# Performance work log

Measured on AMD Instinct MI355X. Metric: run time of the kernel, lower is better.

Reference implementation:

```python
import jax, jax.numpy as jnp
import numpy as np

B = 4; S_L = 512; WIN = 256; SCH = 3; CCH = 128; F = 8; P = 4; RNN = 128; FC = 256
L1 = (WIN - F + 1) // P          # after conv1 + pool1
L2 = (L1 - F + 1) // P           # after conv2 + pool2
D1 = L2 * CCH                    # flattened conv feature dim fed to GRU


def _conv1d(x, w, b):
    # x: (N, W, Cin), w: (F, Cin, Cout), VALID, stride 1 (matches keras Conv1D)
    return jax.lax.conv_general_dilated(x, w, (1,), 'VALID', dimension_numbers=('NWC', 'WIO', 'NWC')) + b


def _maxpool(x, p):
    return jax.lax.reduce_window(x, -jnp.inf, jax.lax.max, (1, p, 1), (1, p, 1), 'VALID')


def _gru(x, h0, mask, W, U, b):
    # keras GRU v2 (reset_after=True). b[0]=input bias, b[1]=recurrent bias.
    # Masked steps carry state through (keras semantics: output==state for GRU).
    u = U.shape[0]
    xg = x @ W + b[0]  # (B, T, 3u) precomputed input projections
    br = b[1]

    def step(h, inp):
        xt, mt = inp  # (B, 3u), (B,)
        rg = h @ U + br
        z = jax.nn.sigmoid(xt[:, :u] + rg[:, :u])
        r = jax.nn.sigmoid(xt[:, u:2 * u] + rg[:, u:2 * u])
        hh = jnp.tanh(xt[:, 2 * u:] + r * rg[:, 2 * u:])
        hn = z * h + (1.0 - z) * hh
        hn = jnp.where(mt[:, None], hn, h)
        return hn, hn

    _, ys = jax.lax.scan(step, h0, (jnp.swapaxes(xg, 0, 1), jnp.swapaxes(mask, 0, 1)))
    return jnp.swapaxes(ys, 0, 1)  # (B, T, u)


def _bidir(x, m, hf, hb, Wf, Uf, bf, Wb, Ub, bb):
    # Bidirectional(merge='concat'); backward layer sees reversed inputs+mask,
    # its output is reversed back to align with time (keras behaviour).
    yf = _gru(x, hf, m, Wf, Uf, bf)
    yb = _gru(x[:, ::-1], hb, m[:, ::-1], Wb, Ub, bb)[:, ::-1]
    return jnp.concatenate([yf, yb], axis=-1)


def _forward(x, state1_f, state1_b, state2_f, state2_b,
             conv1_w, conv1_b, conv2_w, conv2_b,
             g1f_W, g1f_U, g1f_b, g1b_W, g1b_U, g1b_b,
             g2f_W, g2f_U, g2f_b, g2b_W, g2b_U, g2b_b,
             d1_w, d1_b, d2_w, d2_b, d3_w, d3_b, m):
    bsz = x.shape[0]
    h = x.reshape(bsz * S_L, WIN, SCH)
    h = _maxpool(jax.nn.leaky_relu(_conv1d(h, conv1_w, conv1_b), 0.2), P)
    h = _maxpool(jax.nn.leaky_relu(_conv1d(h, conv2_w, conv2_b), 0.2), P)
    h = h.reshape(bsz, S_L, D1)
    h = _bidir(h, m, state1_f, state1_b, g1f_W, g1f_U, g1f_b, g1b_W, g1b_U, g1b_b)
    h = _bidir(h, m, state2_f, state2_b, g2f_W, g2f_U, g2f_b, g2b_W, g2b_U, g2b_b)
    # keras layers.Attention(use_scale=False): dot-product self attention,
    # key mask -> -1e9 on scores, query mask -> zero outputs.
    scores = jnp.einsum('btd,bsd->bts', h, h)
    scores = jnp.where(m[:, None, :], scores, -1e9)
    h = jnp.einsum('bts,bsd->btd', jax.nn.softmax(scores, axis=-1), h)
    h = h * m[:, :, None].astype(h.dtype)
    h = jax.nn.leaky_relu(h @ d1_w + d1_b, 0.2)   # dropout is identity at inference
    h = jax.nn.leaky_relu(h @ d2_w + d2_b, 0.2)
    return (h @ d3_w + d3_b)[..., 0]              # squeeze -> (B, s_l)


def setup_inputs() -> dict:
    key = jax.random.key(0)
    ks = jax.random.split(key, 32)
    g = lambda k, s: jax.random.normal(k, s, jnp.float32) * 0.05
    inp = {}
    inp['x'] = jax.random.normal(ks[0], (B, S_L, WIN, SCH), jnp.float32)
    inp['m'] = jax.random.randint(ks[1], (B, S_L), 0, 2) > 0
    inp['state1_f'] = jax.random.uniform(ks[2], (B, RNN), jnp.float32, -1.0, 1.0)
    inp['state1_b'] = jax.random.uniform(ks[3], (B, RNN), jnp.float32, -1.0, 1.0)
    inp['state2_f'] = jax.random.uniform(ks[4], (B, RNN), jnp.float32, -1.0, 1.0)
    inp['state2_b'] = jax.random.uniform(ks[5], (B, RNN), jnp.float32, -1.0, 1.0)
    inp['conv1_w'] = g(ks[6], (F, SCH, CCH)); inp['conv1_b'] = jnp.zeros((CCH,), jnp.float32)
    inp['conv2_w'] = g(ks[7], (F, CCH, CCH)); inp['conv2_b'] = jnp.zeros((CCH,), jnp.float32)
    i = 8
    for nm, din in (('g1f', D1), ('g1b', D1), ('g2f', 2 * RNN), ('g2b', 2 * RNN)):
        inp[nm + '_W'] = g(ks[i], (din, 3 * RNN))
        inp[nm + '_U'] = g(ks[i + 1], (RNN, 3 * RNN))
        inp[nm + '_b'] = jnp.zeros((2, 3 * RNN), jnp.float32)
        i += 2
    inp['d1_w'] = g(ks[i], (2 * RNN, FC)); inp['d1_b'] = jnp.zeros((FC,), jnp.float32)
    inp['d2_w'] = g(ks[i + 1], (FC, FC)); inp['d2_b'] = jnp.zeros((FC,), jnp.float32)
    inp['d3_w'] = g(ks[i + 2], (FC, 1)); inp['d3_b'] = jnp.zeros((1,), jnp.float32)
    return inp


def reference(x, m, state1_f, state1_b, state2_f, state2_b,
              conv1_w, conv1_b, conv2_w, conv2_b,
              g1f_W, g1f_U, g1f_b, g1b_W, g1b_U, g1b_b,
              g2f_W, g2f_U, g2f_b, g2b_W, g2b_U, g2b_b,
              d1_w, d1_b, d2_w, d2_b, d3_w, d3_b):
    return _forward(x, state1_f, state1_b, state2_f, state2_b,
                    conv1_w, conv1_b, conv2_w, conv2_b,
                    g1f_W, g1f_U, g1f_b, g1b_W, g1b_U, g1b_b,
                    g2f_W, g2f_U, g2f_b, g2b_W, g2b_U, g2b_b,
                    d1_w, d1_b, d2_w, d2_b, d3_w, d3_b, m)
```

## Files before the change

kernel.cpp:

```cpp
#include <hip/hip_runtime.h>

#define LRELU(v) ((v) > 0.f ? (v) : 0.2f * (v))

typedef float f32x4 __attribute__((ext_vector_type(4)));
typedef __bf16 bf16x8 __attribute__((ext_vector_type(8)));
typedef unsigned short ushort8v __attribute__((ext_vector_type(8)));
typedef unsigned int u32x2 __attribute__((ext_vector_type(2)));

__device__ __forceinline__ unsigned short f2bf(float f) {
    unsigned int u = __float_as_uint(f);
    u += 0x7fffu + ((u >> 16) & 1u);
    return (unsigned short)(u >> 16);
}
__device__ __forceinline__ float bf2f(unsigned short h) {
    return __uint_as_float(((unsigned int)h) << 16);
}
__device__ __forceinline__ float sigmoid_fast(float x) {
    float e = __builtin_amdgcn_exp2f(-x * 1.442695041f);
    return __builtin_amdgcn_rcpf(1.f + e);
}
__device__ __forceinline__ float tanh_fast(float x) {
    float e = __builtin_amdgcn_exp2f(x * 2.885390082f);
    return 1.f - 2.f * __builtin_amdgcn_rcpf(e + 1.f);
}
__device__ __forceinline__ float dpp_add_xor1(float v) {
    int r = __builtin_amdgcn_mov_dpp(__float_as_int(v), 0xB1, 0xF, 0xF, true);
    return v + __int_as_float(r);
}
__device__ __forceinline__ float dpp_add_xor2(float v) {
    int r = __builtin_amdgcn_mov_dpp(__float_as_int(v), 0x4E, 0xF, 0xF, true);
    return v + __int_as_float(r);
}

__device__ __forceinline__ void wtpack(const float* __restrict__ W,
                                       unsigned short* __restrict__ h,
                                       unsigned short* __restrict__ l, int K,
                                       int N, long idx) {
    int n = (int)(idx / K), k = (int)(idx % K);
    float v = W[(long)k * N + n];
    unsigned short hi = f2bf(v);
    h[idx] = hi;
    l[idx] = f2bf(v - bf2f(hi));
}
__device__ __forceinline__ void ugpack(const float* __restrict__ U,
                                       float* __restrict__ up, int widx) {
    int quad = widx >> 11;
    int rem = widx & 2047;
    int t = rem >> 2, i = rem & 3;
    int g = quad >> 3, q = quad & 7;
    int c = t >> 2, kq = t & 3;
    up[widx] = U[(long)(kq * 32 + q * 4 + i) * 384 + g * 128 + c];
}

__global__ __launch_bounds__(256) void prepack_all(
    const float* __restrict__ w2, unsigned short* __restrict__ bth,
    unsigned short* __restrict__ btl, const float* __restrict__ g1fW,
    unsigned short* __restrict__ wt1fh, unsigned short* __restrict__ wt1fl,
    const float* __restrict__ g1bW, unsigned short* __restrict__ wt1bh,
    unsigned short* __restrict__ wt1bl, const float* __restrict__ g2fW,
    unsigned short* __restrict__ wt2fh, unsigned short* __restrict__ wt2fl,
    const float* __restrict__ g2bW, unsigned short* __restrict__ wt2bh,
    unsigned short* __restrict__ wt2bl, const float* __restrict__ g1fU,
    float* __restrict__ up1f, const float* __restrict__ g1bU,
    float* __restrict__ up1b, const float* __restrict__ g2fU,
    float* __restrict__ up2f, const float* __restrict__ g2bU,
    float* __restrict__ up2b, const unsigned int* __restrict__ mraw,
    int* __restrict__ mi) {
    const int bid = blockIdx.x, tid = threadIdx.x;
    if (bid < 512) {
        int idx = bid * 256 + tid;
        int c = idx >> 10, k = idx & 1023;
        float v = w2[k * 128 + c];
        unsigned short hi = f2bf(v);
        bth[(long)c * 1024 + k] = hi;
        btl[(long)c * 1024 + k] = f2bf(v - bf2f(hi));
    } else if (bid < 3008) {
        wtpack(g1fW, wt1fh, wt1fl, 1664, 384, (long)(bid - 512) * 256 + tid);
    } else if (bid < 5504) {
        wtpack(g1bW, wt1bh, wt1bl, 1664, 384, (long)(bid - 3008) * 256 + tid);
    } else if (bid < 5888) {
        wtpack(g2fW, wt2fh, wt2fl, 256, 384, (long)(bid - 5504) * 256 + tid);
    } else if (bid < 6272) {
        wtpack(g2bW, wt2bh, wt2bl, 256, 384, (long)(bid - 5888) * 256 + tid);
    } else if (bid < 6464) {
        ugpack(g1fU, up1f, (bid - 6272) * 256 + tid);
    } else if (bid < 6656) {
        ugpack(g1bU, up1b, (bid - 6464) * 256 + tid);
    } else if (bid < 6848) {
        ugpack(g2fU, up2f, (bid - 6656) * 256 + tid);
    } else if (bid < 7040) {
        ugpack(g2bU, up2b, (bid - 6848) * 256 + tid);
    } else {
        __shared__ int flag;
        if (tid == 0) flag = 0;
        __syncthreads();
        unsigned a = mraw[tid * 2], bb = mraw[tid * 2 + 1];
        if (a > 1u || bb > 1u) flag = 1;
        __syncthreads();
        if (flag) {
            const unsigned char* b8 = (const unsigned char*)mraw;
            for (int i = tid; i < 2048; i += 256) mi[i] = b8[i] ? 1 : 0;
        } else {
            for (int i = tid; i < 2048; i += 256) mi[i] = mraw[i] ? 1 : 0;
        }
    }
}

__global__ __launch_bounds__(256) void conv_kernel(
    const float* __restrict__ x, const float* __restrict__ w1,
    const float* __restrict__ b1, const unsigned short* __restrict__ bth,
    const unsigned short* __restrict__ btl, const float* __restrict__ b2,
    unsigned short* __restrict__ feat_h, unsigned short* __restrict__ feat_l) {
    __shared__ float xs[3][256];
    __shared__ __align__(16) unsigned short p1h[72 * 128];
    __shared__ __align__(16) unsigned short p1l[72 * 128];
    long s = blockIdx.x;
    int tid = threadIdx.x;
    const float* xp = x + s * 768;
    for (int i = tid; i < 768; i += 256) xs[i % 3][i / 3] = xp[i];
    for (int i = tid; i < 10 * 128; i += 256) {
        p1h[62 * 128 + i] = 0;
        p1l[62 * 128 + i] = 0;
    }
    __syncthreads();

    {
        int ch = tid & 127;
        int half = tid >> 7;
        float w1r[24];
#pragma unroll
        for (int fc = 0; fc < 24; fc++) w1r[fc] = w1[fc * 128 + ch];
        float bias1 = b1[ch];
        for (int po = half; po < 62; po += 2) {
            int p0 = po * 4;
            float a0 = bias1, a1 = bias1, a2 = bias1, a3 = bias1;
#pragma unroll
            for (int c = 0; c < 3; c++) {
                float xv[11];
#pragma unroll
                for (int q = 0; q < 11; q++) xv[q] = xs[c][p0 + q];
#pragma unroll
                for (int f = 0; f < 8; f++) {
                    float w = w1r[f * 3 + c];
                    a0 = fmaf(xv[f + 0], w, a0);
                    a1 = fmaf(xv[f + 1], w, a1);
                    a2 = fmaf(xv[f + 2], w, a2);
                    a3 = fmaf(xv[f + 3], w, a3);
                }
            }
            float m01 = fmaxf(LRELU(a0), LRELU(a1));
            float m23 = fmaxf(LRELU(a2), LRELU(a3));
            float v = fmaxf(m01, m23);
            unsigned short hi = f2bf(v);
            unsigned short lo = f2bf(v - bf2f(hi));
            int cs = ch ^ ((po & 7) << 3);
            p1h[po * 128 + cs] = hi;
            p1l[po * 128 + cs] = lo;
        }
    }
    __syncthreads();

    const int l = tid & 63, w = tid >> 6;
    const int r = l & 15, g = l >> 4;
    f32x4 acc[4][2];
    const f32x4 zz = {0.f, 0.f, 0.f, 0.f};
#pragma unroll
    for (int m = 0; m < 4; m++) {
        acc[m][0] = zz;
        acc[m][1] = zz;
    }
#pragma unroll 2
    for (int ks = 0; ks < 32; ks++) {
        const int f = ks >> 2;
        const int cin0 = ((ks & 3) << 5) + (g << 3);
        bf16x8 bh[2], bl[2];
#pragma unroll
        for (int n = 0; n < 2; n++) {
            const int c = ((w << 1) + n) * 16 + r;
            const long bo = (long)c * 1024 + (ks << 5) + (g << 3);
            bh[n] = __builtin_bit_cast(bf16x8, *(const ushort8v*)(bth + bo));
            bl[n] = __builtin_bit_cast(bf16x8, *(const ushort8v*)(btl + bo));
        }
        bf16x8 ah[4], al[4];
#pragma unroll
        for (int m = 0; m < 4; m++) {
            const int row = m * 16 + r + f;
            const int col = cin0 ^ ((row & 7) << 3);
            const int off = row * 128 + col;
            ah[m] = __builtin_bit_cast(bf16x8, *(const ushort8v*)(p1h + off));
            al[m] = __builtin_bit_cast(bf16x8, *(const ushort8v*)(p1l + off));
        }
#pragma unroll
        for (int m = 0; m < 4; m++) {
#pragma unroll
            for (int n = 0; n < 2; n++) {
                acc[m][n] = __builtin_amdgcn_mfma_f32_16x16x32_bf16(ah[m], bh[n], acc[m][n], 0, 0, 0);
                acc[m][n] = __builtin_amdgcn_mfma_f32_16x16x32_bf16(ah[m], bl[n], acc[m][n], 0, 0, 0);
                acc[m][n] = __builtin_amdgcn_mfma_f32_16x16x32_bf16(al[m], bh[n], acc[m][n], 0, 0, 0);
            }
        }
    }
#pragma unroll
    for (int m = 0; m < 4; m++) {
        const int j = m * 4 + g;
        if (j < 13) {
#pragma unroll
            for (int n = 0; n < 2; n++) {
                const int ch = ((w << 1) + n) * 16 + r;
                const float bias = b2[ch];
                float v0 = LRELU(acc[m][n].x + bias);
                float v1 = LRELU(acc[m][n].y + bias);
                float v2 = LRELU(acc[m][n].z + bias);
                float v3 = LRELU(acc[m][n].w + bias);
                float v = fmaxf(fmaxf(v0, v1), fmaxf(v2, v3));
                unsigned short hi = f2bf(v);
                feat_h[s * 1664 + j * 128 + ch] = hi;
                feat_l[s * 1664 + j * 128 + ch] = f2bf(v - bf2f(hi));
            }
        }
    }
}

__global__ __launch_bounds__(256) void gemm_proj(
    const unsigned short* __restrict__ Agh, const unsigned short* __restrict__ Agl,
    const unsigned short* __restrict__ B0h, const unsigned short* __restrict__ B0l,
    const unsigned short* __restrict__ B1h, const unsigned short* __restrict__ B1l,
    const float* __restrict__ bias0, const float* __restrict__ bias1,
    float* __restrict__ C0, float* __restrict__ C1, int M, int N, int K) {
    const int z = blockIdx.z;
    const unsigned short* __restrict__ Bth = z ? B1h : B0h;
    const unsigned short* __restrict__ Btl = z ? B1l : B0l;
    const float* __restrict__ bias = z ? bias1 : bias0;
    float* __restrict__ C = z ? C1 : C0;
    __shared__ __align__(16) unsigned short Ahs[2][64 * 32];
    __shared__ __align__(16) unsigned short Als[2][64 * 32];
    const int tid = threadIdx.x;
    const int w = tid >> 6, l = tid & 63, r = l & 15, g = l >> 4;
    const int m0 = blockIdx.y * 64, n0 = blockIdx.x * 64;
    const int col = n0 + w * 16 + r;
    const int srow = tid >> 2, sgq = tid & 3;
    f32x4 acc[4];
    const f32x4 zzv = {0.f, 0.f, 0.f, 0.f};
#pragma unroll
    for (int m = 0; m < 4; m++) acc[m] = zzv;

    const long abase = (long)(m0 + srow) * K + ((sgq ^ (srow & 3)) << 3);
    auto stage = [&](int k0, int buf) {
        __builtin_amdgcn_global_load_lds(
            (const __attribute__((address_space(1))) void*)(Agh + abase + k0),
            (__attribute__((address_space(3))) void*)&Ahs[buf][tid * 8], 16, 0, 0);
        __builtin_amdgcn_global_load_lds(
            (const __attribute__((address_space(1))) void*)(Agl + abase + k0),
            (__attribute__((address_space(3))) void*)&Als[buf][tid * 8], 16, 0, 0);
    };
    stage(0, 0);
    const long bbase = (long)col * K + g * 8;
    ushort8v bhc = *(const ushort8v*)(Bth + bbase);
    ushort8v blc = *(const ushort8v*)(Btl + bbase);

    for (int k0 = 0; k0 < K; k0 += 32) {
        const int buf = (k0 >> 5) & 1;
        asm volatile("s_waitcnt vmcnt(0)" ::: "memory");
        __builtin_amdgcn_s_barrier();
        ushort8v nbh, nbl;
        if (k0 + 32 < K) {
            stage(k0 + 32, buf ^ 1);
            nbh = *(const ushort8v*)(Bth + bbase + k0 + 32);
            nbl = *(const ushort8v*)(Btl + bbase + k0 + 32);
        }
        bf16x8 bh = __builtin_bit_cast(bf16x8, bhc);
        bf16x8 bl = __builtin_bit_cast(bf16x8, blc);
#pragma unroll
        for (int m = 0; m < 4; m++) {
            const int arow = m * 16 + r;
            const int aoff = arow * 32 + ((g ^ (arow & 3)) << 3);
            bf16x8 ah = __builtin_bit_cast(bf16x8, *(const ushort8v*)(&Ahs[buf][aoff]));
            bf16x8 al = __builtin_bit_cast(bf16x8, *(const ushort8v*)(&Als[buf][aoff]));
            acc[m] = __builtin_amdgcn_mfma_f32_16x16x32_bf16(ah, bh, acc[m], 0, 0, 0);
            acc[m] = __builtin_amdgcn_mfma_f32_16x16x32_bf16(ah, bl, acc[m], 0, 0, 0);
            acc[m] = __builtin_amdgcn_mfma_f32_16x16x32_bf16(al, bh, acc[m], 0, 0, 0);
        }
        bhc = nbh;
        blc = nbl;
    }
    const float bv = bias[col];
#pragma unroll
    for (int m = 0; m < 4; m++) {
#pragma unroll
        for (int q = 0; q < 4; q++) {
            const int row = m0 + m * 16 + g * 4 + q;
            C[(long)row * N + col] = acc[m][q] + bv;
        }
    }
}

__global__ __launch_bounds__(256) void gemm_scores(
    const unsigned short* __restrict__ Hh, const unsigned short* __restrict__ Hl,
    const int* __restrict__ mask, float* __restrict__ S) {
    const int bz = blockIdx.z;
    const unsigned short* __restrict__ Agh = Hh + (long)bz * 512 * 256;
    const unsigned short* __restrict__ Agl = Hl + (long)bz * 512 * 256;
    float* __restrict__ C = S + (long)bz * 512 * 512;
    const int K = 256, N = 512;
    __shared__ __align__(16) unsigned short Ahs[2][64 * 32];
    __shared__ __align__(16) unsigned short Als[2][64 * 32];
    const int tid = threadIdx.x;
    const int w = tid >> 6, l = tid & 63, r = l & 15, g = l >> 4;
    const int m0 = blockIdx.y * 64, n0 = blockIdx.x * 64;
    const int col = n0 + w * 16 + r;
    const int srow = tid >> 2, sgq = tid & 3;
    f32x4 acc[4];
    const f32x4 zzv = {0.f, 0.f, 0.f, 0.f};
#pragma unroll
    for (int m = 0; m < 4; m++) acc[m] = zzv;

    const long abase = (long)(m0 + srow) * K + ((sgq ^ (srow & 3)) << 3);
    auto stage = [&](int k0, int buf) {
        __builtin_amdgcn_global_load_lds(
            (const __attribute__((address_space(1))) void*)(Agh + abase + k0),
            (__attribute__((address_space(3))) void*)&Ahs[buf][tid * 8], 16, 0, 0);
        __builtin_amdgcn_global_load_lds(
            (const __attribute__((address_space(1))) void*)(Agl + abase + k0),
            (__attribute__((address_space(3))) void*)&Als[buf][tid * 8], 16, 0, 0);
    };
    stage(0, 0);
    const long bbase = (long)col * K + g * 8;
    ushort8v bhc = *(const ushort8v*)(Agh + bbase);
    ushort8v blc = *(const ushort8v*)(Agl + bbase);

    for (int k0 = 0; k0 < K; k0 += 32) {
        const int buf = (k0 >> 5) & 1;
        asm volatile("s_waitcnt vmcnt(0)" ::: "memory");
        __builtin_amdgcn_s_barrier();
        ushort8v nbh, nbl;
        if (k0 + 32 < K) {
            stage(k0 + 32, buf ^ 1);
            nbh = *(const ushort8v*)(Agh + bbase + k0 + 32);
            nbl = *(const ushort8v*)(Agl + bbase + k0 + 32);
        }
        bf16x8 bh = __builtin_bit_cast(bf16x8, bhc);
        bf16x8 bl = __builtin_bit_cast(bf16x8, blc);
#pragma unroll
        for (int m = 0; m < 4; m++) {
            const int arow = m * 16 + r;
            const int aoff = arow * 32 + ((g ^ (arow & 3)) << 3);
            bf16x8 ah = __builtin_bit_cast(bf16x8, *(const ushort8v*)(&Ahs[buf][aoff]));
            bf16x8 al = __builtin_bit_cast(bf16x8, *(const ushort8v*)(&Als[buf][aoff]));
            acc[m] = __builtin_amdgcn_mfma_f32_16x16x32_bf16(ah, bh, acc[m], 0, 0, 0);
            acc[m] = __builtin_amdgcn_mfma_f32_16x16x32_bf16(ah, bl, acc[m], 0, 0, 0);
            acc[m] = __builtin_amdgcn_mfma_f32_16x16x32_bf16(al, bh, acc[m], 0, 0, 0);
        }
        bhc = nbh;
        blc = nbl;
    }
    const int mk = mask[bz * 512 + col];
#pragma unroll
    for (int m = 0; m < 4; m++) {
#pragma unroll
        for (int q = 0; q < 4; q++) {
            const int row = m0 + m * 16 + g * 4 + q;
            float v = acc[m][q];
            C[(long)row * N + col] = mk ? v : -1e9f;
        }
    }
}

template <int ACT>
__global__ __launch_bounds__(256) void gemm_nn(
    const float* __restrict__ A, long sA, const float* __restrict__ B, long sB,
    const float* __restrict__ bias, const int* __restrict__ qmask,
    float* __restrict__ C, long sC, int M, int N, int K) {
    int bz = blockIdx.z;
    A += (long)bz * sA;
    B += (long)bz * sB;
    C += (long)bz * sC;
    __shared__ __align__(16) float As[16][68];
    __shared__ __align__(16) float Bs[16][68];
    int tid = threadIdx.x;
    int tm = tid >> 4, tn = tid & 15;
    int m0 = blockIdx.y * 64, n0 = blockIdx.x * 64;
    int la_m = tid & 63, la_k = (tid >> 6) * 4;
    int lb_k = tid >> 4, lb_n = (tid & 15) * 4;
    float acc[4][4] = {};
    for (int k0 = 0; k0 < K; k0 += 16) {
        float4 av = *(const float4*)&A[(long)(m0 + la_m) * K + k0 + la_k];
        float4 bv = *(const float4*)&B[(long)(k0 + lb_k) * N + n0 + lb_n];
        As[la_k + 0][la_m] = av.x;
        As[la_k + 1][la_m] = av.y;
        As[la_k + 2][la_m] = av.z;
        As[la_k + 3][la_m] = av.w;
        *(float4*)&Bs[lb_k][lb_n] = bv;
        __syncthreads();
#pragma unroll
        for (int k = 0; k < 16; k++) {
            float4 a4 = *(const float4*)&As[k][tm * 4];
            float4 b4 = *(const float4*)&Bs[k][tn * 4];
            float aa[4] = {a4.x, a4.y, a4.z, a4.w};
            float bb[4] = {b4.x, b4.y, b4.z, b4.w};
#pragma unroll
            for (int i = 0; i < 4; i++)
#pragma unroll
                for (int j = 0; j < 4; j++) acc[i][j] = fmaf(aa[i], bb[j], acc[i][j]);
        }
        __syncthreads();
    }
#pragma unroll
    for (int i = 0; i < 4; i++) {
        int row = m0 + tm * 4 + i;
        float msc = qmask ? (float)qmask[(long)bz * M + row] : 1.f;
#pragma unroll
        for (int j = 0; j < 4; j++) {
            int col = n0 + tn * 4 + j;
            float v = acc[i][j] + (bias ? bias[col] : 0.f);
            if (ACT == 1) v = LRELU(v);
            C[(long)row * N + col] = v * msc;
        }
    }
}

__global__ __launch_bounds__(256) void softmax_kernel(float* __restrict__ S) {
    long row = blockIdx.x;
    float* p = S + row * 512;
    int tid = threadIdx.x;
    __shared__ float red[8];
    float v0 = p[tid], v1 = p[tid + 256];
    float mx = fmaxf(v0, v1);
#pragma unroll
    for (int off = 32; off; off >>= 1) mx = fmaxf(mx, __shfl_down(mx, off));
    if ((tid & 63) == 0) red[tid >> 6] = mx;
    __syncthreads();
    mx = fmaxf(fmaxf(red[0], red[1]), fmaxf(red[2], red[3]));
    float e0 = expf(v0 - mx), e1 = expf(v1 - mx);
    float sm = e0 + e1;
#pragma unroll
    for (int off = 32; off; off >>= 1) sm += __shfl_down(sm, off);
    if ((tid & 63) == 0) red[4 + (tid >> 6)] = sm;
    __syncthreads();
    float inv = 1.f / (red[4] + red[5] + red[6] + red[7]);
    p[tid] = e0 * inv;
    p[tid + 256] = e1 * inv;
}

#define D4(a0, a1, hv, uv)           \
    a0 = fmaf(hv.x, uv.x, a0);       \
    a1 = fmaf(hv.y, uv.y, a1);       \
    a0 = fmaf(hv.z, uv.z, a0);       \
    a1 = fmaf(hv.w, uv.w, a1);

template <int WF32>
__global__ __launch_bounds__(512, 2) void gru_kernel(
    const float* __restrict__ xgf, const float* __restrict__ xgb,
    const float* __restrict__ Upf, const float* __restrict__ Upb,
    const float* __restrict__ brf, const float* __restrict__ brb,
    const float* __restrict__ h0f, const float* __restrict__ h0b,
    const int* __restrict__ mask, float* __restrict__ out,
    unsigned short* __restrict__ outh, unsigned short* __restrict__ outl) {
    int b = blockIdx.x & 3;
    int dir = blockIdx.x >> 2;
    const float* __restrict__ xg = dir ? xgb : xgf;
    const float* __restrict__ Up = dir ? Upb : Upf;
    const float* __restrict__ br = dir ? brb : brf;
    const float* __restrict__ h0 = dir ? h0b : h0f;
    const int tid = threadIdx.x;
    const int c = tid >> 2;
    const int kq = tid & 3;

    __shared__ __align__(16) float xs[2][16 * 384];
    __shared__ __align__(16) float hsh[2][144];
    __shared__ __align__(16) unsigned int histp[16][128];
    __shared__ __align__(16) float histf[16][128];
    __shared__ unsigned long long mwords[8];

    auto stage = [&](int cc, int bufi) {
#pragma unroll
        for (int i = 0; i < 3; i++) {
            int g = i * 512 + tid;
            int j = g / 96;
            int col = (g - j * 96) * 4;
            int ts = cc * 16 + j;
            int t = dir ? (511 - ts) : ts;
            const float* src = xg + ((long)(b * 512 + t)) * 384 + col;
            __builtin_amdgcn_global_load_lds(
                (const __attribute__((address_space(1))) void*)src,
                (__attribute__((address_space(3))) void*)&xs[bufi][g * 4], 16, 0, 0);
        }
    };
    stage(0, 0);

    const float* ub = Up + (tid << 2);
    f32x4 uz0 = *(const f32x4*)(ub + 0 * 2048);
    f32x4 uz1 = *(const f32x4*)(ub + 1 * 2048);
    f32x4 uz2 = *(const f32x4*)(ub + 2 * 2048);
    f32x4 uz3 = *(const f32x4*)(ub + 3 * 2048);
    f32x4 uz4 = *(const f32x4*)(ub + 4 * 2048);
    f32x4 uz5 = *(const f32x4*)(ub + 5 * 2048);
    f32x4 uz6 = *(const f32x4*)(ub + 6 * 2048);
    f32x4 uz7 = *(const f32x4*)(ub + 7 * 2048);
    f32x4 ur0 = *(const f32x4*)(ub + 8 * 2048);
    f32x4 ur1 = *(const f32x4*)(ub + 9 * 2048);
    f32x4 ur2 = *(const f32x4*)(ub + 10 * 2048);
    f32x4 ur3 = *(const f32x4*)(ub + 11 * 2048);
    f32x4 ur4 = *(const f32x4*)(ub + 12 * 2048);
    f32x4 ur5 = *(const f32x4*)(ub + 13 * 2048);
    f32x4 ur6 = *(const f32x4*)(ub + 14 * 2048);
    f32x4 ur7 = *(const f32x4*)(ub + 15 * 2048);
    f32x4 uh0 = *(const f32x4*)(ub + 16 * 2048);
    f32x4 uh1 = *(const f32x4*)(ub + 17 * 2048);
    f32x4 uh2 = *(const f32x4*)(ub + 18 * 2048);
    f32x4 uh3 = *(const f32x4*)(ub + 19 * 2048);
    f32x4 uh4 = *(const f32x4*)(ub + 20 * 2048);
    f32x4 uh5 = *(const f32x4*)(ub + 21 * 2048);
    f32x4 uh6 = *(const f32x4*)(ub + 22 * 2048);
    f32x4 uh7 = *(const f32x4*)(ub + 23 * 2048);

    float br3[3];
#pragma unroll
    for (int g = 0; g < 3; g++) br3[g] = br[g * 128 + c];

    float hreg = h0[b * 128 + c];
    if (kq == 0) hsh[0][c + (c >> 5) * 4] = hreg;
    if (tid < 64) {
#pragma unroll
        for (int w = 0; w < 8; w++) {
            int idx = w * 64 + tid;
            int t = dir ? (511 - idx) : idx;
            unsigned long long bm = __ballot(mask[b * 512 + t] != 0);
            if (tid == 0) mwords[w] = bm;
        }
    }
    asm volatile("s_waitcnt lgkmcnt(0)" ::: "memory");
    __builtin_amdgcn_s_barrier();

    int cur = 0;
    for (int cc = 0; cc < 32; cc++) {
        asm volatile("s_waitcnt vmcnt(0)" ::: "memory");
        if (cc < 31) stage(cc + 1, (cc + 1) & 1);
        __builtin_amdgcn_s_barrier();
        const float* xb = xs[cc & 1];
        unsigned mwbits = (unsigned)((mwords[cc >> 2] >> ((cc & 3) * 16)) & 0xffffull);
#pragma unroll 1
        for (int jj = 0; jj < 16; jj++) {
            if ((mwbits >> jj) & 1) {
                const float* hp = &hsh[cur][kq * 36];
                float4 h0v = *(const float4*)(hp + 0);
                float4 h1v = *(const float4*)(hp + 4);
                float4 h2v = *(const float4*)(hp + 8);
                float4 h3v = *(const float4*)(hp + 12);
                float4 h4v = *(const float4*)(hp + 16);
                float4 h5v = *(const float4*)(hp + 20);
                float4 h6v = *(const float4*)(hp + 24);
                float4 h7v = *(const float4*)(hp + 28);
                float az0 = 0.f, az1 = 0.f, ar0 = 0.f, ar1 = 0.f, ah0 = 0.f, ah1 = 0.f;
                D4(az0, az1, h0v, uz0) D4(az0, az1, h1v, uz1)
                D4(az0, az1, h2v, uz2) D4(az0, az1, h3v, uz3)
                D4(az0, az1, h4v, uz4) D4(az0, az1, h5v, uz5)
                D4(az0, az1, h6v, uz6) D4(az0, az1, h7v, uz7)
                D4(ar0, ar1, h0v, ur0) D4(ar0, ar1, h1v, ur1)
                D4(ar0, ar1, h2v, ur2) D4(ar0, ar1, h3v, ur3)
                D4(ar0, ar1, h4v, ur4) D4(ar0, ar1, h5v, ur5)
                D4(ar0, ar1, h6v, ur6) D4(ar0, ar1, h7v, ur7)
                D4(ah0, ah1, h0v, uh0) D4(ah0, ah1, h1v, uh1)
                D4(ah0, ah1, h2v, uh2) D4(ah0, ah1, h3v, uh3)
                D4(ah0, ah1, h4v, uh4) D4(ah0, ah1, h5v, uh5)
                D4(ah0, ah1, h6v, uh6) D4(ah0, ah1, h7v, uh7)
                float rgz = dpp_add_xor2(dpp_add_xor1(az0 + az1));
                float rgr = dpp_add_xor2(dpp_add_xor1(ar0 + ar1));
                float rgh = dpp_add_xor2(dpp_add_xor1(ah0 + ah1));
                if (kq == 0) {
                    float xz = xb[jj * 384 + c];
                    float xr = xb[jj * 384 + 128 + c];
                    float xh = xb[jj * 384 + 256 + c];
                    float z = sigmoid_fast(xz + rgz + br3[0]);
                    float r_ = sigmoid_fast(xr + rgr + br3[1]);
                    float hc = tanh_fast(fmaf(r_, rgh + br3[2], xh));
                    float hn = fmaf(z, hreg - hc, hc);
                    hreg = hn;
                    hsh[cur ^ 1][c + (c >> 5) * 4] = hn;
                    if (WF32) histf[jj][c] = hn;
                    unsigned short hh = f2bf(hn);
                    histp[jj][c] = (unsigned)hh |
                                   ((unsigned)f2bf(hn - bf2f(hh)) << 16);
                }
                asm volatile("s_waitcnt lgkmcnt(0)" ::: "memory");
                __builtin_amdgcn_s_barrier();
                cur ^= 1;
            } else {
                if (kq == 0) {
                    if (WF32) histf[jj][c] = hreg;
                    unsigned short hh = f2bf(hreg);
                    histp[jj][c] = (unsigned)hh |
                                   ((unsigned)f2bf(hreg - bf2f(hh)) << 16);
                }
            }
        }
        asm volatile("s_waitcnt lgkmcnt(0)" ::: "memory");
        __builtin_amdgcn_s_barrier();
        {
            int fj = tid >> 5, fc = (tid & 31) << 2;
            int ts2 = cc * 16 + fj;
            int tf = dir ? (511 - ts2) : ts2;
            long ob = ((long)(b * 512 + tf)) * 256 + dir * 128 + fc;
            uint4 hp4 = *(const uint4*)&histp[fj][fc];
            u32x2 ph, pl;
            ph.x = (hp4.x & 0xffffu) | (hp4.y << 16);
            ph.y = (hp4.z & 0xffffu) | (hp4.w << 16);
            pl.x = (hp4.x >> 16) | (hp4.y & 0xffff0000u);
            pl.y = (hp4.z >> 16) | (hp4.w & 0xffff0000u);
            *(u32x2*)(outh + ob) = ph;
            *(u32x2*)(outl + ob) = pl;
            if (WF32) *(float4*)(out + ob) = *(const float4*)&histf[fj][fc];
        }
    }
}

__global__ __launch_bounds__(256) void final_kernel(
    const float* __restrict__ fc2, const float* __restrict__ w,
    const float* __restrict__ b, float* __restrict__ out) {
    int row = blockIdx.x * 4 + (threadIdx.x >> 6);
    int lane = threadIdx.x & 63;
    const float* a = fc2 + (long)row * 256;
    float acc = 0.f;
#pragma unroll
    for (int i = 0; i < 4; i++) acc = fmaf(a[lane + i * 64], w[lane + i * 64], acc);
#pragma unroll
    for (int off = 32; off; off >>= 1) acc += __shfl_down(acc, off);
    if (lane == 0) out[row] = acc + b[0];
}

extern "C" void kernel_launch(void* const* d_in, const int* in_sizes, int n_in,
                              void* d_out, int out_size, void* d_ws,
                              size_t ws_size, hipStream_t stream) {
    const float* x = (const float*)d_in[0];
    const unsigned int* mraw = (const unsigned int*)d_in[1];
    const float* s1f = (const float*)d_in[2];
    const float* s1b = (const float*)d_in[3];
    const float* s2f = (const float*)d_in[4];
    const float* s2b = (const float*)d_in[5];
    const float* c1w = (const float*)d_in[6];
    const float* c1b = (const float*)d_in[7];
    const float* c2w = (const float*)d_in[8];
    const float* c2b = (const float*)d_in[9];
    const float* g1fW = (const float*)d_in[10];
    const float* g1fU = (const float*)d_in[11];
    const float* g1fb = (const float*)d_in[12];
    const float* g1bW = (const float*)d_in[13];
    const float* g1bU = (const float*)d_in[14];
    const float* g1bb = (const float*)d_in[15];
    const float* g2fW = (const float*)d_in[16];
    const float* g2fU = (const float*)d_in[17];
    const float* g2fb = (const float*)d_in[18];
    const float* g2bW = (const float*)d_in[19];
    const float* g2bU = (const float*)d_in[20];
    const float* g2bb = (const float*)d_in[21];
    const float* d1w = (const float*)d_in[22];
    const float* d1b = (const float*)d_in[23];
    const float* d2w = (const float*)d_in[24];
    const float* d2b = (const float*)d_in[25];
    const float* d3w = (const float*)d_in[26];
    const float* d3b = (const float*)d_in[27];
    float* out = (float*)d_out;

    float* ws = (float*)d_ws;
    size_t off = 0;
    auto take = [&](size_t n) {
        float* p = ws + off;
        off += (n + 63) & ~(size_t)63;
        return p;
    };
    int* mask_i = (int*)take(2048);
    unsigned short* feat_h = (unsigned short*)take(2048UL * 1664 / 2);
    unsigned short* feat_l = (unsigned short*)take(2048UL * 1664 / 2);
    float* xg1f = take(2048UL * 384);
    float* xg1b = take(2048UL * 384);
    unsigned short* gru1h = (unsigned short*)take(2048UL * 128);
    unsigned short* gru1l = (unsigned short*)take(2048UL * 128);
    float* xg2f = take(2048UL * 384);
    float* xg2b = take(2048UL * 384);
    float* gru2 = take(2048UL * 256);
    unsigned short* gru2h = (unsigned short*)take(2048UL * 128);
    unsigned short* gru2l = (unsigned short*)take(2048UL * 128);
    float* sc = take(4UL * 512 * 512);
    float* attn = take(2048UL * 256);
    float* fc1 = take(2048UL * 256);
    float* fc2 = take(2048UL * 256);
    unsigned short* bth = (unsigned short*)take(65536);
    unsigned short* btl = (unsigned short*)take(65536);
    unsigned short* wt1fh = (unsigned short*)take(319488);
    unsigned short* wt1fl = (unsigned short*)take(319488);
    unsigned short* wt1bh = (unsigned short*)take(319488);
    unsigned short* wt1bl = (unsigned short*)take(319488);
    unsigned short* wt2fh = (unsigned short*)take(49152);
    unsigned short* wt2fl = (unsigned short*)take(49152);
    unsigned short* wt2bh = (unsigned short*)take(49152);
    unsigned short* wt2bl = (unsigned short*)take(49152);
    float* up1f = take(49152);
    float* up1b = take(49152);
    float* up2f = take(49152);
    float* up2b = take(49152);

    prepack_all<<<7041, 256, 0, stream>>>(
        c2w, bth, btl, g1fW, wt1fh, wt1fl, g1bW, wt1bh, wt1bl, g2fW, wt2fh,
        wt2fl, g2bW, wt2bh, wt2bl, g1fU, up1f, g1bU, up1b, g2fU, up2f, g2bU,
        up2b, mraw, mask_i);
    conv_kernel<<<2048, 256, 0, stream>>>(x, c1w, c1b, bth, btl, c2b, feat_h, feat_l);

    gemm_proj<<<dim3(6, 32, 2), 256, 0, stream>>>(
        feat_h, feat_l, wt1fh, wt1fl, wt1bh, wt1bl, g1fb, g1bb, xg1f, xg1b,
        2048, 384, 1664);
    gru_kernel<0><<<8, 512, 0, stream>>>(xg1f, xg1b, up1f, up1b, g1fb + 384,
                                         g1bb + 384, s1f, s1b, mask_i, nullptr,
                                         gru1h, gru1l);

    gemm_proj<<<dim3(6, 32, 2), 256, 0, stream>>>(
        gru1h, gru1l, wt2fh, wt2fl, wt2bh, wt2bl, g2fb, g2bb, xg2f, xg2b,
        2048, 384, 256);
    gru_kernel<1><<<8, 512, 0, stream>>>(xg2f, xg2b, up2f, up2b, g2fb + 384,
                                         g2bb + 384, s2f, s2b, mask_i, gru2,
                                         gru2h, gru2l);

    gemm_scores<<<dim3(8, 8, 4), 256, 0, stream>>>(gru2h, gru2l, mask_i, sc);
    softmax_kernel<<<2048, 256, 0, stream>>>(sc);
    gemm_nn<0><<<dim3(4, 8, 4), 256, 0, stream>>>(sc, 512L * 512, gru2, 512L * 256,
                                                  nullptr, mask_i, attn, 512L * 256,
                                                  512, 256, 512);

    gemm_nn<1><<<dim3(4, 32, 1), 256, 0, stream>>>(attn, 0, d1w, 0, d1b, nullptr,
                                                   fc1, 0, 2048, 256, 256);
    gemm_nn<1><<<dim3(4, 32, 1), 256, 0, stream>>>(fc1, 0, d2w, 0, d2b, nullptr,
                                                   fc2, 0, 2048, 256, 256);
    final_kernel<<<512, 256, 0, stream>>>(fc2, d3w, d3b, out);
}
```

Baseline: 669.1 us.

## Move attention and dense GEMMs to split-bf16 MFMA with hi/lo activations

Replaces the three FP32 SIMT gemm_nn launches (attention-weighted sum and two dense layers) with an MFMA kernel that uses split bf16 hi/lo operands and three MFMAs per tile for near-FP32 accuracy. Softmax, the dense layers and the final reduction now produce and consume bf16 hi/lo pairs, and the GRU no longer writes an FP32 history copy. A new transpose kernel and extra prepack blocks lay out the GRU output and dense weights as K-major B operands. This trades scalar FMA throughput for matrix-core throughput, with small extra rounding error and one more kernel launch.

After: 630.5 us, median of 2. 1.06x faster.

```diff
diff --git a/kernel.cpp b/kernel.cpp
--- a/kernel.cpp
+++ b/kernel.cpp
@@ -64,7 +64,10 @@
     float* __restrict__ up1f, const float* __restrict__ g1bU,
     float* __restrict__ up1b, const float* __restrict__ g2fU,
     float* __restrict__ up2f, const float* __restrict__ g2bU,
-    float* __restrict__ up2b, const unsigned int* __restrict__ mraw,
+    float* __restrict__ up2b, const float* __restrict__ d1w,
+    unsigned short* __restrict__ d1th, unsigned short* __restrict__ d1tl,
+    const float* __restrict__ d2w, unsigned short* __restrict__ d2th,
+    unsigned short* __restrict__ d2tl, const unsigned int* __restrict__ mraw,
     int* __restrict__ mi) {
     const int bid = blockIdx.x, tid = threadIdx.x;
     if (bid < 512) {
@@ -90,6 +93,10 @@
         ugpack(g2fU, up2f, (bid - 6656) * 256 + tid);
     } else if (bid < 7040) {
         ugpack(g2bU, up2b, (bid - 6848) * 256 + tid);
+    } else if (bid < 7296) {
+        wtpack(d1w, d1th, d1tl, 256, 256, (long)(bid - 7040) * 256 + tid);
+    } else if (bid < 7552) {
+        wtpack(d2w, d2th, d2tl, 256, 256, (long)(bid - 7296) * 256 + tid);
     } else {
         __shared__ int flag;
         if (tid == 0) flag = 0;
@@ -365,62 +372,118 @@
     }
 }
 
-template <int ACT>
-__global__ __launch_bounds__(256) void gemm_nn(
-    const float* __restrict__ A, long sA, const float* __restrict__ B, long sB,
+template <int ACT, int QMASK>
+__global__ __launch_bounds__(256) void gemm_v3(
+    const unsigned short* __restrict__ Agh, const unsigned short* __restrict__ Agl,
+    const unsigned short* __restrict__ Bth, const unsigned short* __restrict__ Btl,
     const float* __restrict__ bias, const int* __restrict__ qmask,
-    float* __restrict__ C, long sC, int M, int N, int K) {
-    int bz = blockIdx.z;
-    A += (long)bz * sA;
-    B += (long)bz * sB;
-    C += (long)bz * sC;
-    __shared__ __align__(16) float As[16][68];
-    __shared__ __align__(16) float Bs[16][68];
-    int tid = threadIdx.x;
-    int tm = tid >> 4, tn = tid & 15;
-    int m0 = blockIdx.y * 64, n0 = blockIdx.x * 64;
-    int la_m = tid & 63, la_k = (tid >> 6) * 4;
-    int lb_k = tid >> 4, lb_n = (tid & 15) * 4;
-    float acc[4][4] = {};
-    for (int k0 = 0; k0 < K; k0 += 16) {
-        float4 av = *(const float4*)&A[(long)(m0 + la_m) * K + k0 + la_k];
-        float4 bv = *(const float4*)&B[(long)(k0 + lb_k) * N + n0 + lb_n];
-        As[la_k + 0][la_m] = av.x;
-        As[la_k + 1][la_m] = av.y;
-        As[la_k + 2][la_m] = av.z;
-        As[la_k + 3][la_m] = av.w;
-        *(float4*)&Bs[lb_k][lb_n] = bv;
-        __syncthreads();
-#pragma unroll
-        for (int k = 0; k < 16; k++) {
-            float4 a4 = *(const float4*)&As[k][tm * 4];
-            float4 b4 = *(const float4*)&Bs[k][tn * 4];
-            float aa[4] = {a4.x, a4.y, a4.z, a4.w};
-            float bb[4] = {b4.x, b4.y, b4.z, b4.w};
-#pragma unroll
-            for (int i = 0; i < 4; i++)
-#pragma unroll
-                for (int j = 0; j < 4; j++) acc[i][j] = fmaf(aa[i], bb[j], acc[i][j]);
-        }
-        __syncthreads();
-    }
+    unsigned short* __restrict__ Ch, unsigned short* __restrict__ Cl,
+    long sA, long sB, long sC, int M, int N, int K) {
+    const int bz = blockIdx.z;
+    Agh += (long)bz * sA;
+    Agl += (long)bz * sA;
+    Bth += (long)bz * sB;
+    Btl += (long)bz * sB;
+    Ch += (long)bz * sC;
+    Cl += (long)bz * sC;
+    __shared__ __align__(16) unsigned short Ahs[2][64 * 32];
+    __shared__ __align__(16) unsigned short Als[2][64 * 32];
+    const int tid = threadIdx.x;
+    const int w = tid >> 6, l = tid & 63, r = l & 15, g = l >> 4;
+    const int m0 = blockIdx.y * 64, n0 = blockIdx.x * 64;
+    const int col = n0 + w * 16 + r;
+    const int srow = tid >> 2, sgq = tid & 3;
+    f32x4 acc[4];
+    const f32x4 zzv = {0.f, 0.f, 0.f, 0.f};
+#pragma unroll
+    for (int m = 0; m < 4; m++) acc[m] = zzv;
+
+    const long abase = (long)(m0 + srow) * K + ((sgq ^ (srow & 3)) << 3);
+    auto stage = [&](int k0, int buf) {
+        __builtin_amdgcn_global_load_lds(
+            (const __attribute__((address_space(1))) void*)(Agh + abase + k0),
+            (__attribute__((address_space(3))) void*)&Ahs[buf][tid * 8], 16, 0, 0);
+        __builtin_amdgcn_global_load_lds(
+            (const __attribute__((address_space(1))) void*)(Agl + abase + k0),
+            (__attribute__((address_space(3))) void*)&Als[buf][tid * 8], 16, 0, 0);
+    };
+    stage(0, 0);
+    const long bbase = (long)col * K + g * 8;
+    ushort8v bhc = *(const ushort8v*)(Bth + bbase);
+    ushort8v blc = *(const ushort8v*)(Btl + bbase);
+
+    for (int k0 = 0; k0 < K; k0 += 32) {
+        const int buf = (k0 >> 5) & 1;
+        asm volatile("s_waitcnt vmcnt(0)" ::: "memory");
+        __builtin_amdgcn_s_barrier();
+        ushort8v nbh, nbl;
+        if (k0 + 32 < K) {
+            stage(k0 + 32, buf ^ 1);
+            nbh = *(const ushort8v*)(Bth + bbase + k0 + 32);
+            nbl = *(const ushort8v*)(Btl + bbase + k0 + 32);
+        }
+        bf16x8 bh = __builtin_bit_cast(bf16x8, bhc);
+        bf16x8 bl = __builtin_bit_cast(bf16x8, blc);
+#pragma unroll
+        for (int m = 0; m < 4; m++) {
+            const int arow = m * 16 + r;
+            const int aoff = arow * 32 + ((g ^ (arow & 3)) << 3);
+            bf16x8 ah = __builtin_bit_cast(bf16x8, *(const ushort8v*)(&Ahs[buf][aoff]));
+            bf16x8 al = __builtin_bit_cast(bf16x8, *(const ushort8v*)(&Als[buf][aoff]));
+            acc[m] = __builtin_amdgcn_mfma_f32_16x16x32_bf16(ah, bh, acc[m], 0, 0, 0);
+            acc[m] = __builtin_amdgcn_mfma_f32_16x16x32_bf16(ah, bl, acc[m], 0, 0, 0);
+            acc[m] = __builtin_amdgcn_mfma_f32_16x16x32_bf16(al, bh, acc[m], 0, 0, 0);
+        }
+        bhc = nbh;
+        blc = nbl;
+    }
+    const float bv = bias ? bias[col] : 0.f;
+#pragma unroll
+    for (int m = 0; m < 4; m++) {
+#pragma unroll
+        for (int q = 0; q < 4; q++) {
+            const int row = m0 + m * 16 + g * 4 + q;
+            float v = acc[m][q] + bv;
+            if (ACT == 1) v = LRELU(v);
+            if (QMASK) v *= (float)qmask[bz * M + row];
+            unsigned short hi = f2bf(v);
+            Ch[(long)row * N + col] = hi;
+            Cl[(long)row * N + col] = f2bf(v - bf2f(hi));
+        }
+    }
+}
+
+__global__ __launch_bounds__(256) void transpose_hl(
+    const unsigned short* __restrict__ inh, const unsigned short* __restrict__ inl,
+    unsigned short* __restrict__ outh, unsigned short* __restrict__ outl) {
+    __shared__ unsigned short th[32][33], tl[32][33];
+    const int b = blockIdx.z;
+    const int s0 = blockIdx.x * 32, d0 = blockIdx.y * 32;
+    const unsigned short* ih = inh + (long)b * 512 * 256;
+    const unsigned short* il = inl + (long)b * 512 * 256;
+    unsigned short* oh = outh + (long)b * 256 * 512;
+    unsigned short* ol = outl + (long)b * 256 * 512;
+    const int tx = threadIdx.x & 31, ty = threadIdx.x >> 5;
 #pragma unroll
     for (int i = 0; i < 4; i++) {
-        int row = m0 + tm * 4 + i;
-        float msc = qmask ? (float)qmask[(long)bz * M + row] : 1.f;
-#pragma unroll
-        for (int j = 0; j < 4; j++) {
-            int col = n0 + tn * 4 + j;
-            float v = acc[i][j] + (bias ? bias[col] : 0.f);
-            if (ACT == 1) v = LRELU(v);
-            C[(long)row * N + col] = v * msc;
-        }
-    }
-}
-
-__global__ __launch_bounds__(256) void softmax_kernel(float* __restrict__ S) {
+        int s = s0 + ty + i * 8;
+        th[ty + i * 8][tx] = ih[(long)s * 256 + d0 + tx];
+        tl[ty + i * 8][tx] = il[(long)s * 256 + d0 + tx];
+    }
+    __syncthreads();
+#pragma unroll
+    for (int i = 0; i < 4; i++) {
+        int d = d0 + ty + i * 8;
+        oh[(long)d * 512 + s0 + tx] = th[tx][ty + i * 8];
+        ol[(long)d * 512 + s0 + tx] = tl[tx][ty + i * 8];
+    }
+}
+
+__global__ __launch_bounds__(256) void softmax_kernel(
+    const float* __restrict__ S, unsigned short* __restrict__ Ph,
+    unsigned short* __restrict__ Pl) {
     long row = blockIdx.x;
-    float* p = S + row * 512;
+    const float* p = S + row * 512;
     int tid = threadIdx.x;
     __shared__ float red[8];
     float v0 = p[tid], v1 = p[tid + 256];
@@ -437,8 +500,12 @@
     if ((tid & 63) == 0) red[4 + (tid >> 6)] = sm;
     __syncthreads();
     float inv = 1.f / (red[4] + red[5] + red[6] + red[7]);
-    p[tid] = e0 * inv;
-    p[tid + 256] = e1 * inv;
+    float w0 = e0 * inv, w1 = e1 * inv;
+    unsigned short h0 = f2bf(w0), h1 = f2bf(w1);
+    Ph[row * 512 + tid] = h0;
+    Pl[row * 512 + tid] = f2bf(w0 - bf2f(h0));
+    Ph[row * 512 + tid + 256] = h1;
+    Pl[row * 512 + tid + 256] = f2bf(w1 - bf2f(h1));
 }
 
 #define D4(a0, a1, hv, uv)           \
@@ -447,14 +514,13 @@
     a0 = fmaf(hv.z, uv.z, a0);       \
     a1 = fmaf(hv.w, uv.w, a1);
 
-template <int WF32>
 __global__ __launch_bounds__(512, 2) void gru_kernel(
     const float* __restrict__ xgf, const float* __restrict__ xgb,
     const float* __restrict__ Upf, const float* __restrict__ Upb,
     const float* __restrict__ brf, const float* __restrict__ brb,
     const float* __restrict__ h0f, const float* __restrict__ h0b,
-    const int* __restrict__ mask, float* __restrict__ out,
-    unsigned short* __restrict__ outh, unsigned short* __restrict__ outl) {
+    const int* __restrict__ mask, unsigned short* __restrict__ outh,
+    unsigned short* __restrict__ outl) {
     int b = blockIdx.x & 3;
     int dir = blockIdx.x >> 2;
     const float* __restrict__ xg = dir ? xgb : xgf;
@@ -468,7 +534,6 @@
     __shared__ __align__(16) float xs[2][16 * 384];
     __shared__ __align__(16) float hsh[2][144];
     __shared__ __align__(16) unsigned int histp[16][128];
-    __shared__ __align__(16) float histf[16][128];
     __shared__ unsigned long long mwords[8];
 
     auto stage = [&](int cc, int bufi) {
@@ -576,7 +641,6 @@
                     float hn = fmaf(z, hreg - hc, hc);
                     hreg = hn;
                     hsh[cur ^ 1][c + (c >> 5) * 4] = hn;
-                    if (WF32) histf[jj][c] = hn;
                     unsigned short hh = f2bf(hn);
                     histp[jj][c] = (unsigned)hh |
                                    ((unsigned)f2bf(hn - bf2f(hh)) << 16);
@@ -586,7 +650,6 @@
                 cur ^= 1;
             } else {
                 if (kq == 0) {
-                    if (WF32) histf[jj][c] = hreg;
                     unsigned short hh = f2bf(hreg);
                     histp[jj][c] = (unsigned)hh |
                                    ((unsigned)f2bf(hreg - bf2f(hh)) << 16);
@@ -608,20 +671,25 @@
             pl.y = (hp4.z >> 16) | (hp4.w & 0xffff0000u);
             *(u32x2*)(outh + ob) = ph;
             *(u32x2*)(outl + ob) = pl;
-            if (WF32) *(float4*)(out + ob) = *(const float4*)&histf[fj][fc];
         }
     }
 }
 
 __global__ __launch_bounds__(256) void final_kernel(
-    const float* __restrict__ fc2, const float* __restrict__ w,
-    const float* __restrict__ b, float* __restrict__ out) {
+    const unsigned short* __restrict__ fh, const unsigned short* __restrict__ fl,
+    const float* __restrict__ w, const float* __restrict__ b,
+    float* __restrict__ out) {
     int row = blockIdx.x * 4 + (threadIdx.x >> 6);
     int lane = threadIdx.x & 63;
-    const float* a = fc2 + (long)row * 256;
+    const unsigned short* ah = fh + (long)row * 256;
+    const unsigned short* al = fl + (long)row * 256;
     float acc = 0.f;
 #pragma unroll
-    for (int i = 0; i < 4; i++) acc = fmaf(a[lane + i * 64], w[lane + i * 64], acc);
+    for (int i = 0; i < 4; i++) {
+        int idx = lane + i * 64;
+        float a = bf2f(ah[idx]) + bf2f(al[idx]);
+        acc = fmaf(a, w[idx], acc);
+    }
 #pragma unroll
     for (int off = 32; off; off >>= 1) acc += __shfl_down(acc, off);
     if (lane == 0) out[row] = acc + b[0];
@@ -676,13 +744,19 @@
     unsigned short* gru1l = (unsigned short*)take(2048UL * 128);
     float* xg2f = take(2048UL * 384);
     float* xg2b = take(2048UL * 384);
-    float* gru2 = take(2048UL * 256);
     unsigned short* gru2h = (unsigned short*)take(2048UL * 128);
     unsigned short* gru2l = (unsigned short*)take(2048UL * 128);
+    unsigned short* ght = (unsigned short*)take(2048UL * 128);
+    unsigned short* glt = (unsigned short*)take(2048UL * 128);
     float* sc = take(4UL * 512 * 512);
-    float* attn = take(2048UL * 256);
-    float* fc1 = take(2048UL * 256);
-    float* fc2 = take(2048UL * 256);
+    unsigned short* scH = (unsigned short*)take(4UL * 512 * 256);
+    unsigned short* scL = (unsigned short*)take(4UL * 512 * 256);
+    unsigned short* attnH = (unsigned short*)take(2048UL * 128);
+    unsigned short* attnL = (unsigned short*)take(2048UL * 128);
+    unsigned short* fc1H = (unsigned short*)take(2048UL * 128);
+    unsigned short* fc1L = (unsigned short*)take(2048UL * 128);
+    unsigned short* fc2H = (unsigned short*)take(2048UL * 128);
+    unsigned short* fc2L = (unsigned short*)take(2048UL * 128);
     unsigned short* bth = (unsigned short*)take(65536);
     unsigned short* btl = (unsigned short*)take(65536);
     unsigned short* wt1fh = (unsigned short*)take(319488);
@@ -693,40 +767,44 @@
     unsigned short* wt2fl = (unsigned short*)take(49152);
     unsigned short* wt2bh = (unsigned short*)take(49152);
     unsigned short* wt2bl = (unsigned short*)take(49152);
+    unsigned short* d1th = (unsigned short*)take(32768);
+    unsigned short* d1tl = (unsigned short*)take(32768);
+    unsigned short* d2th = (unsigned short*)take(32768);
+    unsigned short* d2tl = (unsigned short*)take(32768);
     float* up1f = take(49152);
     float* up1b = take(49152);
     float* up2f = take(49152);
     float* up2b = take(49152);
 
-    prepack_all<<<7041, 256, 0, stream>>>(
+    prepack_all<<<7553, 256, 0, stream>>>(
         c2w, bth, btl, g1fW, wt1fh, wt1fl, g1bW, wt1bh, wt1bl, g2fW, wt2fh,
         wt2fl, g2bW, wt2bh, wt2bl, g1fU, up1f, g1bU, up1b, g2fU, up2f, g2bU,
-        up2b, mraw, mask_i);
+        up2b, d1w, d1th, d1tl, d2w, d2th, d2tl, mraw, mask_i);
     conv_kernel<<<2048, 256, 0, stream>>>(x, c1w, c1b, bth, btl, c2b, feat_h, feat_l);
 
     gemm_proj<<<dim3(6, 32, 2), 256, 0, stream>>>(
         feat_h, feat_l, wt1fh, wt1fl, wt1bh, wt1bl, g1fb, g1bb, xg1f, xg1b,
         2048, 384, 1664);
-    gru_kernel<0><<<8, 512, 0, stream>>>(xg1f, xg1b, up1f, up1b, g1fb + 384,
-                                         g1bb + 384, s1f, s1b, mask_i, nullptr,
-                                         gru1h, gru1l);
+    gru_kernel<<<8, 512, 0, stream>>>(xg1f, xg1b, up1f, up1b, g1fb + 384,
+                                      g1bb + 384, s1f, s1b, mask_i, gru1h, gru1l);
 
     gemm_proj<<<dim3(6, 32, 2), 256, 0, stream>>>(
         gru1h, gru1l, wt2fh, wt2fl, wt2bh, wt2bl, g2fb, g2bb, xg2f, xg2b,
         2048, 384, 256);
-    gru_kernel<1><<<8, 512, 0, stream>>>(xg2f, xg2b, up2f, up2b, g2fb + 384,
-                                         g2bb + 384, s2f, s2b, mask_i, gru2,
-                                         gru2h, gru2l);
-
+    gru_kernel<<<8, 512, 0, stream>>>(xg2f, xg2b, up2f, up2b, g2fb + 384,
+                                      g2bb + 384, s2f, s2b, mask_i, gru2h, gru2l);
+
+    transpose_hl<<<dim3(16, 8, 4), 256, 0, stream>>>(gru2h, gru2l, ght, glt);
     gemm_scores<<<dim3(8, 8, 4), 256, 0, stream>>>(gru2h, gru2l, mask_i, sc);
-    softmax_kernel<<<2048, 256, 0, stream>>>(sc);
-    gemm_nn<0><<<dim3(4, 8, 4), 256, 0, stream>>>(sc, 512L * 512, gru2, 512L * 256,
-                                                  nullptr, mask_i, attn, 512L * 256,
-                                                  512, 256, 512);
-
-    gemm_nn<1><<<dim3(4, 32, 1), 256, 0, stream>>>(attn, 0, d1w, 0, d1b, nullptr,
-                                                   fc1, 0, 2048, 256, 256);
-    gemm_nn<1><<<dim3(4, 32, 1), 256, 0, stream>>>(fc1, 0, d2w, 0, d2b, nullptr,
-                                                   fc2, 0, 2048, 256, 256);
-    final_kernel<<<512, 256, 0, stream>>>(fc2, d3w, d3b, out);
-}
+    softmax_kernel<<<2048, 256, 0, stream>>>(sc, scH, scL);
+    gemm_v3<0, 1><<<dim3(4, 8, 4), 256, 0, stream>>>(
+        scH, scL, ght, glt, nullptr, mask_i, attnH, attnL,
+        512L * 512, 256L * 512, 512L * 256, 512, 256, 512);
+    gemm_v3<1, 0><<<dim3(4, 32, 1), 256, 0, stream>>>(
+        attnH, attnL, d1th, d1tl, d1b, nullptr, fc1H, fc1L,
+        0, 0, 0, 2048, 256, 256);
+    gemm_v3<1, 0><<<dim3(4, 32, 1), 256, 0, stream>>>(
+        fc1H, fc1L, d2th, d2tl, d2b, nullptr, fc2H, fc2L,
+        0, 0, 0, 2048, 256, 256);
+    final_kernel<<<512, 256, 0, stream>>>(fc2H, fc2L, d3w, d3b, out);
+}
```
